# Kernel tuning notes

Hardware: AMD Instinct MI355X
Metric: run time of the kernel (lower is better)

The kernel has to match this reference:

```python
import jax, jax.numpy as jnp
import numpy as np

N_TOKENS = 16384
D_IN = 1024
D_OUT = 1024
N_EXPS = 8


def setup_inputs() -> dict:
    key = jax.random.key(0)
    k1, k2, k3, k4 = jax.random.split(key, 4)
    embs = jax.random.normal(k1, (N_TOKENS, D_IN), dtype=jnp.float32)
    exps_T = jax.random.normal(k2, (D_IN, N_EXPS), dtype=jnp.float32) * 0.02
    expert_bias = jax.random.normal(k3, (N_EXPS, D_IN), dtype=jnp.float32) * 0.02
    expert_W = jax.random.normal(k4, (N_EXPS, D_OUT, D_IN), dtype=jnp.float32) * 0.02
    return {"embs": embs, "exps_T": exps_T, "expert_bias": expert_bias, "expert_W": expert_W}


def reference(embs, exps_T, expert_bias, expert_W):
    # Gating (eval path: no noise, no rel_gate)
    scores = embs @ exps_T                      # [n, e]
    exps_sco = jax.nn.softmax(scores, axis=-1)  # [n, e]
    # All-experts dense evaluation: (embs - bias_e) @ W_e^T for each expert e
    shifted = embs[:, None, :] - expert_bias[None, :, :]        # [n, e, d]
    expert_outputs = jnp.einsum('ned,eod->neo', shifted, expert_W)  # [n, e, o]
    # Softmax-weighted reduction over experts
    multi_out = jnp.einsum('ne,neo->no', exps_sco, expert_outputs)  # [n, o]
    return (multi_out, expert_outputs)
```

## Files before the change

kernel.cpp:

```cpp
#include <hip/hip_runtime.h>
#include <hip/hip_bf16.h>
#include <stdint.h>

#define N_TOKENS 16384
#define D_IN 1024
#define D_OUT 1024
#define N_EXPS 8

typedef __bf16 bf16x8 __attribute__((ext_vector_type(8)));
typedef float f32x4 __attribute__((ext_vector_type(4)));

typedef __attribute__((address_space(1))) void gvoid_t;
typedef __attribute__((address_space(3))) void lvoid_t;

__device__ __forceinline__ void async_copy16(void* lds, const void* g) {
    __builtin_amdgcn_global_load_lds((gvoid_t*)g, (lvoid_t*)lds, 16, 0, 0);
}

__device__ __forceinline__ unsigned short f2bf_u16(float f) {
    union { __hip_bfloat16 h; unsigned short u; } cv;
    cv.h = __float2bfloat16(f);
    return cv.u;
}

__global__ __launch_bounds__(256) void gate_convert_kernel(
    const float* __restrict__ embs, const float* __restrict__ expsT,
    unsigned short* __restrict__ embs_bf, float* __restrict__ probs) {
    const int row  = blockIdx.x * 4 + (threadIdx.x >> 6);
    const int lane = threadIdx.x & 63;
    const float* er = embs + (size_t)row * D_IN;

    float s[N_EXPS];
#pragma unroll
    for (int e = 0; e < N_EXPS; ++e) s[e] = 0.f;

#pragma unroll
    for (int j = 0; j < 4; ++j) {
        const int chunk = j * 64 + lane;
        const float4 v = ((const float4*)er)[chunk];
        const int d = chunk * 4;
        const float vv[4] = {v.x, v.y, v.z, v.w};
#pragma unroll
        for (int q = 0; q < 4; ++q) {
            const float4 t0 = ((const float4*)(expsT + (size_t)(d + q) * N_EXPS))[0];
            const float4 t1 = ((const float4*)(expsT + (size_t)(d + q) * N_EXPS))[1];
            s[0] += vv[q] * t0.x; s[1] += vv[q] * t0.y;
            s[2] += vv[q] * t0.z; s[3] += vv[q] * t0.w;
            s[4] += vv[q] * t1.x; s[5] += vv[q] * t1.y;
            s[6] += vv[q] * t1.z; s[7] += vv[q] * t1.w;
        }
        ushort4 u;
        u.x = f2bf_u16(v.x); u.y = f2bf_u16(v.y);
        u.z = f2bf_u16(v.z); u.w = f2bf_u16(v.w);
        ((ushort4*)embs_bf)[(size_t)row * 256 + chunk] = u;
    }

#pragma unroll
    for (int off = 32; off; off >>= 1) {
#pragma unroll
        for (int e = 0; e < N_EXPS; ++e) s[e] += __shfl_xor(s[e], off, 64);
    }

    float mx = s[0];
#pragma unroll
    for (int e = 1; e < N_EXPS; ++e) mx = fmaxf(mx, s[e]);
    float pe[N_EXPS];
    float sum = 0.f;
#pragma unroll
    for (int e = 0; e < N_EXPS; ++e) { pe[e] = __expf(s[e] - mx); sum += pe[e]; }
    const float inv = 1.f / sum;
    if (lane == 0) {
#pragma unroll
        for (int e = 0; e < N_EXPS; ++e) probs[(size_t)row * N_EXPS + e] = pe[e] * inv;
    }
}

__global__ __launch_bounds__(256) void wconv_kernel(
    const float* __restrict__ W, const float* __restrict__ bias,
    unsigned short* __restrict__ Wbf, float* __restrict__ cvec) {
    const int gw   = blockIdx.x * 4 + (threadIdx.x >> 6);
    const int lane = threadIdx.x & 63;
    const int e    = gw >> 10;
    const float* wr = W + (size_t)gw * D_IN;
    const float* br = bias + (size_t)e * D_IN;

    float dot = 0.f;
#pragma unroll
    for (int j = 0; j < 4; ++j) {
        const int chunk = j * 64 + lane;
        const float4 w4 = ((const float4*)wr)[chunk];
        const float4 b4 = ((const float4*)br)[chunk];
        dot += w4.x * b4.x + w4.y * b4.y + w4.z * b4.z + w4.w * b4.w;
        ushort4 u;
        u.x = f2bf_u16(w4.x); u.y = f2bf_u16(w4.y);
        u.z = f2bf_u16(w4.z); u.w = f2bf_u16(w4.w);
        ((ushort4*)Wbf)[(size_t)gw * 256 + chunk] = u;
    }
#pragma unroll
    for (int off = 32; off; off >>= 1) dot += __shfl_xor(dot, off, 64);
    if (lane == 0) cvec[gw] = dot;
}

__global__ __launch_bounds__(256, 2) void moe_gemm_kernel(
    const __hip_bfloat16* __restrict__ Abf, const __hip_bfloat16* __restrict__ Wbf,
    const float* __restrict__ probs, const float* __restrict__ cvec,
    float* __restrict__ out_multi, float* __restrict__ out_exp) {
    constexpr int BM = 128, BN = 128, BK = 32;
    __shared__ __align__(16) __hip_bfloat16 As[BM * BK];
    __shared__ __align__(16) __hip_bfloat16 Bs[2][BN * BK];
    __shared__ float p_lds[N_EXPS][BM];
    __shared__ float c_lds[N_EXPS][BN];

    const int tid  = threadIdx.x;
    const int lane = tid & 63;
    const int lm   = lane & 15;
    const int lq   = lane >> 4;
    const int wave = tid >> 6;
    const int wm   = (wave >> 1) * 64;
    const int wn   = (wave & 1) * 64;
    const int nT   = blockIdx.x & 7;
    const int mT   = blockIdx.x >> 3;
    const int m0   = mT * BM;
    const int n0   = nT * BN;

    for (int i = tid; i < N_EXPS * BM; i += 256)
        p_lds[i >> 7][i & 127] = probs[(size_t)(m0 + (i & 127)) * N_EXPS + (i >> 7)];
    for (int i = tid; i < N_EXPS * BN; i += 256)
        c_lds[i >> 7][i & 127] = cvec[(size_t)(i >> 7) * D_OUT + n0 + (i & 127)];

    const int c0 = tid, c1 = 256 + tid;
    const __hip_bfloat16* gA0 = Abf + (size_t)(m0 + (c0 >> 2)) * D_IN + (c0 & 3) * 8;
    const __hip_bfloat16* gA1 = Abf + (size_t)(m0 + (c1 >> 2)) * D_IN + (c1 & 3) * 8;
    const __hip_bfloat16* gB0 = Wbf + (size_t)(n0 + (c0 >> 2)) * D_IN + (c0 & 3) * 8;
    const __hip_bfloat16* gB1 = Wbf + (size_t)(n0 + (c1 >> 2)) * D_IN + (c1 & 3) * 8;
    __hip_bfloat16* lA0  = As + (tid & ~63) * 8;
    __hip_bfloat16* lA1  = lA0 + 2048;
    __hip_bfloat16* lB00 = Bs[0] + (tid & ~63) * 8;
    __hip_bfloat16* lB01 = lB00 + 2048;
    __hip_bfloat16* lB10 = Bs[1] + (tid & ~63) * 8;
    __hip_bfloat16* lB11 = lB10 + 2048;

    const int abase = (wm + lm) * BK + lq * 8;
    const int bbase = (wn + lm) * BK + lq * 8;

    float multi[4][4][4];
#pragma unroll
    for (int ti = 0; ti < 4; ++ti)
#pragma unroll
        for (int tj = 0; tj < 4; ++tj)
#pragma unroll
            for (int r = 0; r < 4; ++r) multi[ti][tj][r] = 0.f;

    const f32x4 fzero = {0.f, 0.f, 0.f, 0.f};

    auto epilogue = [&](int e, f32x4 (&acc)[4][4]) {
        float cv[4];
#pragma unroll
        for (int tj = 0; tj < 4; ++tj) cv[tj] = c_lds[e][wn + tj * 16 + lm];
#pragma unroll
        for (int ti = 0; ti < 4; ++ti) {
#pragma unroll
            for (int r = 0; r < 4; ++r) {
                const int rloc = wm + ti * 16 + lq * 4 + r;
                const int grow = m0 + rloc;
                const float p = p_lds[e][rloc];
                float* orow = out_exp + ((size_t)grow * N_EXPS + e) * D_OUT + n0 + wn;
#pragma unroll
                for (int tj = 0; tj < 4; ++tj) {
                    const float val = acc[ti][tj][r] - cv[tj];
                    __builtin_nontemporal_store(val, &orow[tj * 16 + lm]);
                    multi[ti][tj][r] = fmaf(p, val, multi[ti][tj][r]);
                }
            }
        }
    };

    for (int ep = 0; ep < N_EXPS / 2; ++ep) {
        const int e0 = 2 * ep, e1 = 2 * ep + 1;
        const size_t e0off = (size_t)e0 * D_OUT * D_IN;
        const size_t e1off = (size_t)e1 * D_OUT * D_IN;
        f32x4 acc0[4][4], acc1[4][4];
#pragma unroll
        for (int ti = 0; ti < 4; ++ti)
#pragma unroll
            for (int tj = 0; tj < 4; ++tj) { acc0[ti][tj] = fzero; acc1[ti][tj] = fzero; }

        for (int kt = 0; kt < D_IN / BK; ++kt) {
            const int ko = kt * BK;
            async_copy16(lA0,  gA0 + ko);
            async_copy16(lA1,  gA1 + ko);
            async_copy16(lB00, gB0 + e0off + ko);
            async_copy16(lB01, gB1 + e0off + ko);
            async_copy16(lB10, gB0 + e1off + ko);
            async_copy16(lB11, gB1 + e1off + ko);
            __syncthreads();

            bf16x8 a[4], b[4];
#pragma unroll
            for (int t = 0; t < 4; ++t) a[t] = *(const bf16x8*)(As + abase + t * 16 * BK);
#pragma unroll
            for (int t = 0; t < 4; ++t) b[t] = *(const bf16x8*)(Bs[0] + bbase + t * 16 * BK);
#pragma unroll
            for (int ti = 0; ti < 4; ++ti)
#pragma unroll
                for (int tj = 0; tj < 4; ++tj)
                    acc0[ti][tj] = __builtin_amdgcn_mfma_f32_16x16x32_bf16(
                        a[ti], b[tj], acc0[ti][tj], 0, 0, 0);
#pragma unroll
            for (int t = 0; t < 4; ++t) b[t] = *(const bf16x8*)(Bs[1] + bbase + t * 16 * BK);
#pragma unroll
            for (int ti = 0; ti < 4; ++ti)
#pragma unroll
                for (int tj = 0; tj < 4; ++tj)
                    acc1[ti][tj] = __builtin_amdgcn_mfma_f32_16x16x32_bf16(
                        a[ti], b[tj], acc1[ti][tj], 0, 0, 0);
            __syncthreads();
        }

        epilogue(e0, acc0);
        epilogue(e1, acc1);
    }

#pragma unroll
    for (int ti = 0; ti < 4; ++ti) {
#pragma unroll
        for (int r = 0; r < 4; ++r) {
            const int grow = m0 + wm + ti * 16 + lq * 4 + r;
            float* mrow = out_multi + (size_t)grow * D_OUT + n0 + wn;
#pragma unroll
            for (int tj = 0; tj < 4; ++tj)
                __builtin_nontemporal_store(multi[ti][tj][r], &mrow[tj * 16 + lm]);
        }
    }
}

extern "C" void kernel_launch(void* const* d_in, const int* in_sizes, int n_in,
                              void* d_out, int out_size, void* d_ws, size_t ws_size,
                              hipStream_t stream) {
    const float* embs  = (const float*)d_in[0];
    const float* expsT = (const float*)d_in[1];
    const float* bias  = (const float*)d_in[2];
    const float* W     = (const float*)d_in[3];

    float* out_multi = (float*)d_out;
    float* out_exp   = (float*)d_out + (size_t)N_TOKENS * D_OUT;

    char* ws = (char*)d_ws;
    unsigned short* embs_bf = (unsigned short*)ws;
    unsigned short* W_bf    = (unsigned short*)(ws + 33554432);
    float*          probs   = (float*)(ws + 33554432 + 16777216);
    float*          cvec    = (float*)(ws + 33554432 + 16777216 + 524288);

    gate_convert_kernel<<<N_TOKENS / 4, 256, 0, stream>>>(embs, expsT, embs_bf, probs);
    wconv_kernel<<<(N_EXPS * D_OUT) / 4, 256, 0, stream>>>(W, bias, W_bf, cvec);
    moe_gemm_kernel<<<(N_TOKENS / 128) * (D_OUT / 128), 256, 0, stream>>>(
        (const __hip_bfloat16*)embs_bf, (const __hip_bfloat16*)W_bf,
        probs, cvec, out_multi, out_exp);
}
```

Baseline: 960.7 us.

## Double-buffer LDS tiles and prefetch next K-step across a flattened expert loop

Doubles the A and B LDS buffers and issues the async global-to-LDS copies for the next K-step before computing the current one. The loop over expert pairs and K-steps is flattened into one 128-iteration loop, so prefetching continues across expert boundaries and through the epilogue. Explicit vmcnt waits and s_barriers replace the two __syncthreads. The aim is to hide global-load latency behind the MFMA work, at the cost of more LDS per block (which may pressure occupancy) and a dependence on hand-written waitcnt counts being correct.

```diff
diff --git a/kernel.cpp b/kernel.cpp
--- a/kernel.cpp
+++ b/kernel.cpp
@@ -106,8 +106,8 @@
     const float* __restrict__ probs, const float* __restrict__ cvec,
     float* __restrict__ out_multi, float* __restrict__ out_exp) {
     constexpr int BM = 128, BN = 128, BK = 32;
-    __shared__ __align__(16) __hip_bfloat16 As[BM * BK];
-    __shared__ __align__(16) __hip_bfloat16 Bs[2][BN * BK];
+    __shared__ __align__(16) __hip_bfloat16 As[2][BM * BK];
+    __shared__ __align__(16) __hip_bfloat16 Bs[2][2][BN * BK];
     __shared__ float p_lds[N_EXPS][BM];
     __shared__ float c_lds[N_EXPS][BN];
 
@@ -123,22 +123,36 @@
     const int m0   = mT * BM;
     const int n0   = nT * BN;
 
-    for (int i = tid; i < N_EXPS * BM; i += 256)
-        p_lds[i >> 7][i & 127] = probs[(size_t)(m0 + (i & 127)) * N_EXPS + (i >> 7)];
-    for (int i = tid; i < N_EXPS * BN; i += 256)
-        c_lds[i >> 7][i & 127] = cvec[(size_t)(i >> 7) * D_OUT + n0 + (i & 127)];
-
     const int c0 = tid, c1 = 256 + tid;
     const __hip_bfloat16* gA0 = Abf + (size_t)(m0 + (c0 >> 2)) * D_IN + (c0 & 3) * 8;
     const __hip_bfloat16* gA1 = Abf + (size_t)(m0 + (c1 >> 2)) * D_IN + (c1 & 3) * 8;
     const __hip_bfloat16* gB0 = Wbf + (size_t)(n0 + (c0 >> 2)) * D_IN + (c0 & 3) * 8;
     const __hip_bfloat16* gB1 = Wbf + (size_t)(n0 + (c1 >> 2)) * D_IN + (c1 & 3) * 8;
-    __hip_bfloat16* lA0  = As + (tid & ~63) * 8;
-    __hip_bfloat16* lA1  = lA0 + 2048;
-    __hip_bfloat16* lB00 = Bs[0] + (tid & ~63) * 8;
-    __hip_bfloat16* lB01 = lB00 + 2048;
-    __hip_bfloat16* lB10 = Bs[1] + (tid & ~63) * 8;
-    __hip_bfloat16* lB11 = lB10 + 2048;
+    const int wbase = (tid & ~63) * 8;
+
+    auto stage = [&](int it) {
+        const int b  = it & 1;
+        const int kt = it & 31;
+        const int ep = it >> 5;
+        const int ko = kt * BK;
+        const size_t e0off = (size_t)(2 * ep) * ((size_t)D_OUT * D_IN);
+        const size_t e1off = e0off + (size_t)D_OUT * D_IN;
+        __hip_bfloat16* lA  = &As[b][0] + wbase;
+        __hip_bfloat16* lB0 = &Bs[b][0][0] + wbase;
+        __hip_bfloat16* lB1 = &Bs[b][1][0] + wbase;
+        async_copy16(lA,         gA0 + ko);
+        async_copy16(lA + 2048,  gA1 + ko);
+        async_copy16(lB0,        gB0 + e0off + ko);
+        async_copy16(lB0 + 2048, gB1 + e0off + ko);
+        async_copy16(lB1,        gB0 + e1off + ko);
+        async_copy16(lB1 + 2048, gB1 + e1off + ko);
+    };
+    stage(0);
+
+    for (int i = tid; i < N_EXPS * BM; i += 256)
+        p_lds[i >> 7][i & 127] = probs[(size_t)(m0 + (i & 127)) * N_EXPS + (i >> 7)];
+    for (int i = tid; i < N_EXPS * BN; i += 256)
+        c_lds[i >> 7][i & 127] = cvec[(size_t)(i >> 7) * D_OUT + n0 + (i & 127)];
 
     const int abase = (wm + lm) * BK + lq * 8;
     const int bbase = (wn + lm) * BK + lq * 8;
@@ -175,50 +189,58 @@
         }
     };
 
-    for (int ep = 0; ep < N_EXPS / 2; ++ep) {
-        const int e0 = 2 * ep, e1 = 2 * ep + 1;
-        const size_t e0off = (size_t)e0 * D_OUT * D_IN;
-        const size_t e1off = (size_t)e1 * D_OUT * D_IN;
-        f32x4 acc0[4][4], acc1[4][4];
+    f32x4 acc0[4][4], acc1[4][4];
+#pragma unroll
+    for (int ti = 0; ti < 4; ++ti)
+#pragma unroll
+        for (int tj = 0; tj < 4; ++tj) { acc0[ti][tj] = fzero; acc1[ti][tj] = fzero; }
+
+    for (int it = 0; it < 4 * 32; ++it) {
+        const int cur = it & 1;
+        if (it < 127) {
+            stage(it + 1);
+            asm volatile("s_waitcnt vmcnt(6)" ::: "memory");
+        } else {
+            asm volatile("s_waitcnt vmcnt(0)" ::: "memory");
+        }
+        __builtin_amdgcn_s_barrier();
+        __builtin_amdgcn_sched_barrier(0);
+
+        const __hip_bfloat16* Ac  = &As[cur][0];
+        const __hip_bfloat16* Bc0 = &Bs[cur][0][0];
+        const __hip_bfloat16* Bc1 = &Bs[cur][1][0];
+        bf16x8 a[4], b[4];
+#pragma unroll
+        for (int t = 0; t < 4; ++t) a[t] = *(const bf16x8*)(Ac + abase + t * 16 * BK);
+#pragma unroll
+        for (int t = 0; t < 4; ++t) b[t] = *(const bf16x8*)(Bc0 + bbase + t * 16 * BK);
 #pragma unroll
         for (int ti = 0; ti < 4; ++ti)
 #pragma unroll
-            for (int tj = 0; tj < 4; ++tj) { acc0[ti][tj] = fzero; acc1[ti][tj] = fzero; }
-
-        for (int kt = 0; kt < D_IN / BK; ++kt) {
-            const int ko = kt * BK;
-            async_copy16(lA0,  gA0 + ko);
-            async_copy16(lA1,  gA1 + ko);
-            async_copy16(lB00, gB0 + e0off + ko);
-            async_copy16(lB01, gB1 + e0off + ko);
-            async_copy16(lB10, gB0 + e1off + ko);
-            async_copy16(lB11, gB1 + e1off + ko);
-            __syncthreads();
-
-            bf16x8 a[4], b[4];
-#pragma unroll
-            for (int t = 0; t < 4; ++t) a[t] = *(const bf16x8*)(As + abase + t * 16 * BK);
-#pragma unroll
-            for (int t = 0; t < 4; ++t) b[t] = *(const bf16x8*)(Bs[0] + bbase + t * 16 * BK);
+            for (int tj = 0; tj < 4; ++tj)
+                acc0[ti][tj] = __builtin_amdgcn_mfma_f32_16x16x32_bf16(
+                    a[ti], b[tj], acc0[ti][tj], 0, 0, 0);
+#pragma unroll
+        for (int t = 0; t < 4; ++t) b[t] = *(const bf16x8*)(Bc1 + bbase + t * 16 * BK);
+#pragma unroll
+        for (int ti = 0; ti < 4; ++ti)
+#pragma unroll
+            for (int tj = 0; tj < 4; ++tj)
+                acc1[ti][tj] = __builtin_amdgcn_mfma_f32_16x16x32_bf16(
+                    a[ti], b[tj], acc1[ti][tj], 0, 0, 0);
+
+        __builtin_amdgcn_sched_barrier(0);
+        __builtin_amdgcn_s_barrier();
+
+        if ((it & 31) == 31) {
+            const int e0 = 2 * (it >> 5);
+            epilogue(e0, acc0);
+            epilogue(e0 + 1, acc1);
 #pragma unroll
             for (int ti = 0; ti < 4; ++ti)
 #pragma unroll
-                for (int tj = 0; tj < 4; ++tj)
-                    acc0[ti][tj] = __builtin_amdgcn_mfma_f32_16x16x32_bf16(
-                        a[ti], b[tj], acc0[ti][tj], 0, 0, 0);
-#pragma unroll
-            for (int t = 0; t < 4; ++t) b[t] = *(const bf16x8*)(Bs[1] + bbase + t * 16 * BK);
-#pragma unroll
-            for (int ti = 0; ti < 4; ++ti)
-#pragma unroll
-                for (int tj = 0; tj < 4; ++tj)
-                    acc1[ti][tj] = __builtin_amdgcn_mfma_f32_16x16x32_bf16(
-                        a[ti], b[tj], acc1[ti][tj], 0, 0, 0);
-            __syncthreads();
-        }
-
-        epilogue(e0, acc0);
-        epilogue(e1, acc1);
+                for (int tj = 0; tj < 4; ++tj) { acc0[ti][tj] = fzero; acc1[ti][tj] = fzero; }
+        }
     }
 
 #pragma unroll
```

Measured after the change: 975.2 us. Within noise of the previous version (+1.5%).
